# Optimization experiments

Measured on AMD Instinct MI355X. Metric: run time of the kernel, lower is better.

Reference implementation:

```python
import math
import jax, jax.numpy as jnp
import numpy as np

L, D, H, F, V, S = 4, 1024, 16, 4096, 50257, 2048
HS = D // H
EPS = 1e-5
STD = 0.02


def setup_inputs() -> dict:
    key = jax.random.key(0)
    keys = iter(jax.random.split(key, 24))

    def rn(shape):
        return (jax.random.normal(next(keys), shape, jnp.float32) * STD)

    inp = {
        "input_ids": jax.random.randint(next(keys), (1, S), 0, V, dtype=jnp.int64),
        "tok_emb": rn((V, D)),
        "pos_emb": rn((S, D)),
        # per-layer stacked params; linear weights stored [in, out]
        "Wq": rn((L, D, D)), "bq": jnp.zeros((L, D)),
        "Wk": rn((L, D, D)), "bk": jnp.zeros((L, D)),
        "Wv": rn((L, D, D)), "bv": jnp.zeros((L, D)),
        "Wo": rn((L, D, D)), "bo": jnp.zeros((L, D)),
        "W1": rn((L, D, F)), "b1": jnp.zeros((L, F)),
        "W2": rn((L, F, D)), "b2": jnp.zeros((L, D)),
        "ln1w": jnp.ones((L, D)), "ln1b": jnp.zeros((L, D)),
        "ln2w": jnp.ones((L, D)), "ln2b": jnp.zeros((L, D)),
        "lnfw": jnp.ones((D,)), "lnfb": jnp.zeros((D,)),
        "lm_head": rn((V, D)),  # torch Linear weight layout [out, in]
    }
    return inp


def _layernorm(x, w, b):
    m = jnp.mean(x, axis=-1, keepdims=True)
    v = jnp.mean(jnp.square(x - m), axis=-1, keepdims=True)
    return (x - m) * jax.lax.rsqrt(v + EPS) * w + b


def reference(input_ids, tok_emb, pos_emb, Wq, bq, Wk, bk, Wv, bv, Wo, bo,
              W1, b1, W2, b2, ln1w, ln1b, ln2w, ln2b, lnfw, lnfb, lm_head):
    B, Sq = input_ids.shape
    h = tok_emb[input_ids] + pos_emb[None, :Sq]  # [B,S,D]
    causal = jnp.tril(jnp.ones((Sq, Sq), dtype=bool))
    scale = 1.0 / math.sqrt(HS)

    def block(h, p):
        wq, bq_, wk, bk_, wv, bv_, wo, bo_, w1, b1_, w2, b2_, l1w, l1b, l2w, l2b = p
        x = _layernorm(h, l1w, l1b)
        q = (x @ wq + bq_).reshape(B, Sq, H, HS).transpose(0, 2, 1, 3)
        k = (x @ wk + bk_).reshape(B, Sq, H, HS).transpose(0, 2, 1, 3)
        v = (x @ wv + bv_).reshape(B, Sq, H, HS).transpose(0, 2, 1, 3)
        scores = jnp.einsum('bhqd,bhkd->bhqk', q, k) * scale
        scores = jnp.where(causal, scores, jnp.finfo(scores.dtype).min)
        attn = jax.nn.softmax(scores, axis=-1)  # dropout is identity at eval
        out = jnp.einsum('bhqk,bhkd->bhqd', attn, v)
        out = out.transpose(0, 2, 1, 3).reshape(B, Sq, D)
        h = h + out @ wo + bo_
        x = _layernorm(h, l2w, l2b)
        h = h + jax.nn.gelu(x @ w1 + b1_, approximate=False) @ w2 + b2_
        return h, None

    h, _ = jax.lax.scan(block, h, (Wq, bq, Wk, bk, Wv, bv, Wo, bo,
                                   W1, b1, W2, b2, ln1w, ln1b, ln2w, ln2b))
    h = _layernorm(h, lnfw, lnfb)
    logits = h @ lm_head.T  # [B,S,V]
    return logits
```

## Files before the change

kernel.cpp:

```cpp
#include <hip/hip_runtime.h>
#include <math.h>
#include <stdint.h>


#define SEQ 2048
#define DIM 1024
#define NHEAD 16
#define FFN 4096
#define VOCAB 50257
#define NLAYER 4
#define LNEPS 1e-5f
#define QKVD 3072
#define KVB 128

using bf16x8 = __attribute__((ext_vector_type(8))) short;
using s16x4  = __attribute__((ext_vector_type(4))) short;
using f32x4  = __attribute__((ext_vector_type(4))) float;
using fl4    = __attribute__((ext_vector_type(4))) float;

static __device__ __forceinline__ short f2bf(float f) {
  uint32_t u = __float_as_uint(f);
  u = (u + 0x7fffu + ((u >> 16) & 1u)) >> 16;
  return (short)u;
}
static __device__ __forceinline__ float bf2f(short s) {
  return __uint_as_float(((uint32_t)(uint16_t)s) << 16);
}
static __device__ __forceinline__ void gload_lds16(const void* g, void* l) {
  __builtin_amdgcn_global_load_lds((const __attribute__((address_space(1))) void*)g,
                                   (__attribute__((address_space(3))) void*)l, 16, 0, 0);
}

__global__ void embed_kernel(const int* __restrict__ ids,
                             const float* __restrict__ tok,
                             const float* __restrict__ pos,
                             float* __restrict__ h) {
  int i = blockIdx.x * blockDim.x + threadIdx.x;
  if (i < SEQ * DIM) {
    int s = i / DIM, d = i % DIM;
    h[i] = tok[(long)ids[s] * DIM + d] + pos[i];
  }
}

__global__ void ln_kernel(const float* __restrict__ x, const float* __restrict__ w,
                          const float* __restrict__ b, short* __restrict__ y) {
  int row = blockIdx.x;
  const float* xr = x + (long)row * DIM;
  short* yr = y + (long)row * DIM;
  int tid = threadIdx.x;
  float v0 = xr[tid], v1 = xr[tid + 256], v2 = xr[tid + 512], v3 = xr[tid + 768];
  __shared__ float red[8];
  float s = v0 + v1 + v2 + v3;
#pragma unroll
  for (int o = 32; o >= 1; o >>= 1) s += __shfl_xor(s, o);
  if ((tid & 63) == 0) red[tid >> 6] = s;
  __syncthreads();
  float mean = (red[0] + red[1] + red[2] + red[3]) * (1.f / DIM);
  float d0 = v0 - mean, d1 = v1 - mean, d2 = v2 - mean, d3 = v3 - mean;
  float q = d0 * d0 + d1 * d1 + d2 * d2 + d3 * d3;
#pragma unroll
  for (int o = 32; o >= 1; o >>= 1) q += __shfl_xor(q, o);
  if ((tid & 63) == 0) red[4 + (tid >> 6)] = q;
  __syncthreads();
  float var = (red[4] + red[5] + red[6] + red[7]) * (1.f / DIM);
  float rstd = rsqrtf(var + LNEPS);
  yr[tid]       = f2bf(d0 * rstd * w[tid] + b[tid]);
  yr[tid + 256] = f2bf(d1 * rstd * w[tid + 256] + b[tid + 256]);
  yr[tid + 512] = f2bf(d2 * rstd * w[tid + 512] + b[tid + 512]);
  yr[tid + 768] = f2bf(d3 * rstd * w[tid + 768] + b[tid + 768]);
}

__global__ void transpose_w(const float* __restrict__ in, short* __restrict__ out,
                            int K, int N) {
  __shared__ float t[32][33];
  int c0 = blockIdx.x * 32, r0 = blockIdx.y * 32;
  int tx = threadIdx.x & 31, ty = threadIdx.x >> 5;
#pragma unroll
  for (int i = 0; i < 4; i++)
    t[ty + i * 8][tx] = in[(long)(r0 + ty + i * 8) * N + c0 + tx];
  __syncthreads();
#pragma unroll
  for (int i = 0; i < 4; i++)
    out[(long)(c0 + ty + i * 8) * K + r0 + tx] = f2bf(t[tx][ty + i * 8]);
}

struct TW4 { const float* src[4]; short* dst[4]; };
__global__ void transpose_w4(TW4 p) {
  const float* in = p.src[blockIdx.z];
  short* out = p.dst[blockIdx.z];
  __shared__ float t[32][33];
  int c0 = blockIdx.x * 32, r0 = blockIdx.y * 32;
  int tx = threadIdx.x & 31, ty = threadIdx.x >> 5;
#pragma unroll
  for (int i = 0; i < 4; i++)
    t[ty + i * 8][tx] = in[(long)(r0 + ty + i * 8) * DIM + c0 + tx];
  __syncthreads();
#pragma unroll
  for (int i = 0; i < 4; i++)
    out[(long)(c0 + ty + i * 8) * DIM + r0 + tx] = f2bf(t[tx][ty + i * 8]);
}

__global__ void transpose_v(const short* __restrict__ qkv, short* __restrict__ vt) {
  __shared__ short t[64][72];
  int s0 = blockIdx.x * 64, c0 = blockIdx.y * 64;
  int tid = threadIdx.x;
#pragma unroll
  for (int i = 0; i < 2; i++) {
    int ca = i * 256 + tid;
    int row = ca >> 3, cp = ca & 7;
    bf16x8 v = *(const bf16x8*)(qkv + (long)(s0 + row) * QKVD + 2 * DIM + c0 + cp * 8);
    *(bf16x8*)&t[row][cp * 8] = v;
  }
  __syncthreads();
#pragma unroll
  for (int i = 0; i < 2; i++) {
    int ca = i * 256 + tid;
    int crow = ca >> 3, sp = ca & 7;
    s16x4 a, b;
#pragma unroll
    for (int u = 0; u < 4; u++) a[u] = t[sp * 8 + u][crow];
#pragma unroll
    for (int u = 0; u < 4; u++) b[u] = t[sp * 8 + 4 + u][crow];
    bf16x8 o;
#pragma unroll
    for (int u = 0; u < 4; u++) { o[u] = a[u]; o[4 + u] = b[u]; }
    *(bf16x8*)(vt + (long)(c0 + crow) * SEQ + s0 + sp * 8) = o;
  }
}

__global__ void conv_bf16(const float* __restrict__ in, short* __restrict__ out, long n4) {
  long i = (long)blockIdx.x * blockDim.x + threadIdx.x;
  long stride = (long)gridDim.x * blockDim.x;
  for (; i < n4; i += stride) {
    fl4 v = *(const fl4*)(in + i * 4);
    s16x4 o;
    o[0] = f2bf(v[0]); o[1] = f2bf(v[1]); o[2] = f2bf(v[2]); o[3] = f2bf(v[3]);
    *(s16x4*)(out + i * 4) = o;
  }
}

__global__ void bias_cat(const float* __restrict__ bq, const float* __restrict__ bk,
                         const float* __restrict__ bv, float* __restrict__ out) {
  int i = blockIdx.x * 256 + threadIdx.x;
  if (i < QKVD) out[i] = i < DIM ? bq[i] : (i < 2 * DIM ? bk[i - DIM] : bv[i - 2 * DIM]);
}

template <bool XCDSWZ>
__global__ __launch_bounds__(512, 2) void gemm256(
    const short* __restrict__ A, const short* __restrict__ Bt,
    float* __restrict__ C, int N, int K) {
  __shared__ short ldsA[2][256 * 64];
  __shared__ short ldsB[2][256 * 64];
  const int tid = threadIdx.x, wid = tid >> 6, lane = tid & 63;
  const int l16 = lane & 15, lg = lane >> 4;
  const int wm = wid >> 2, wn = wid & 3;
  int bx = blockIdx.x, by = blockIdx.y;
  if (XCDSWZ) {
    int gx = gridDim.x, nwg = gx * gridDim.y;
    int flat = by * gx + bx;
    int nf = (flat & 7) * (nwg >> 3) + (flat >> 3);
    bx = nf % gx; by = nf / gx;
  }
  const long m0 = (long)bx * 256, n0 = (long)by * 256;
  const int NT = K / 64;

  auto SA = [&](int t, int b, int r0) {
    int row = r0 + wid * 8 + (lane >> 3);
    int c = (lane & 7) ^ (row & 7);
    gload_lds16(A + (m0 + row) * (long)K + t * 64 + c * 8,
                &ldsA[b][(r0 + wid * 8) * 64]);
  };
  auto SB = [&](int t, int b, int r0) {
    int row = r0 + wid * 8 + (lane >> 3);
    int c = (lane & 7) ^ (row & 7);
    int rowb = (int)n0 + row;
    if (rowb > N - 1) rowb = N - 1;
    gload_lds16(Bt + (long)rowb * K + t * 64 + c * 8,
                &ldsB[b][(r0 + wid * 8) * 64]);
  };

  f32x4 acc[8][4] = {};
  bf16x8 bfr[4][2];

  auto PH = [&](int b, int q) {
    bf16x8 af[2][2];
    if (q == 0) {
#pragma unroll
      for (int nf = 0; nf < 4; nf++) {
        int row = wn * 64 + nf * 16 + l16;
#pragma unroll
        for (int ks = 0; ks < 2; ks++)
          bfr[nf][ks] = *(const bf16x8*)((const char*)&ldsB[b][0] + row * 128 +
                                         (((ks * 4 + lg) ^ (row & 7)) * 16));
      }
    }
#pragma unroll
    for (int j = 0; j < 2; j++) {
      int row = wm * 128 + (q * 2 + j) * 16 + l16;
#pragma unroll
      for (int ks = 0; ks < 2; ks++)
        af[j][ks] = *(const bf16x8*)((const char*)&ldsA[b][0] + row * 128 +
                                     (((ks * 4 + lg) ^ (row & 7)) * 16));
    }
    __builtin_amdgcn_s_barrier();
    __builtin_amdgcn_s_setprio(1);
#pragma unroll
    for (int ks = 0; ks < 2; ks++)
#pragma unroll
      for (int j = 0; j < 2; j++)
#pragma unroll
        for (int nf = 0; nf < 4; nf++)
          acc[q * 2 + j][nf] =
              __builtin_amdgcn_mfma_f32_16x16x32_bf16(af[j][ks], bfr[nf][ks],
                                                      acc[q * 2 + j][nf], 0, 0, 0);
    __builtin_amdgcn_s_setprio(0);
  };

  SA(0, 0, 0); SA(0, 0, 64); SA(0, 0, 128); SA(0, 0, 192);
  SB(0, 0, 0); SB(0, 0, 64); SB(0, 0, 128); SB(0, 0, 192);
  SA(1, 1, 0); SA(1, 1, 128);
  asm volatile("s_waitcnt vmcnt(2)" ::: "memory");
  __builtin_amdgcn_s_barrier();

  for (int i = 0; i < NT / 2; i++) {
    const int e = 2 * i, o = e + 1;
    const bool more = (e + 2) < NT;
    SA(o, 1, 64); SA(o, 1, 192);
    PH(0, 0);
    __builtin_amdgcn_s_barrier();
    SB(o, 1, 0); SB(o, 1, 64);
    PH(0, 1);
    __builtin_amdgcn_s_barrier();
    SB(o, 1, 128); SB(o, 1, 192);
    PH(0, 2);
    __builtin_amdgcn_s_barrier();
    if (more) { SA(e + 2, 0, 0); SA(e + 2, 0, 128); }
    PH(0, 3);
    if (more) asm volatile("s_waitcnt vmcnt(2)" ::: "memory");
    else      asm volatile("s_waitcnt vmcnt(0)" ::: "memory");
    __builtin_amdgcn_s_barrier();
    if (more) { SA(e + 2, 0, 64); SA(e + 2, 0, 192); }
    PH(1, 0);
    __builtin_amdgcn_s_barrier();
    if (more) { SB(e + 2, 0, 0); SB(e + 2, 0, 64); }
    PH(1, 1);
    __builtin_amdgcn_s_barrier();
    if (more) { SB(e + 2, 0, 128); SB(e + 2, 0, 192); }
    PH(1, 2);
    __builtin_amdgcn_s_barrier();
    if (more) { SA(e + 3, 1, 0); SA(e + 3, 1, 128); }
    PH(1, 3);
    if (more) {
      asm volatile("s_waitcnt vmcnt(2)" ::: "memory");
      __builtin_amdgcn_s_barrier();
    }
  }

#pragma unroll
  for (int mf = 0; mf < 8; mf++)
#pragma unroll
    for (int nf = 0; nf < 4; nf++)
#pragma unroll
      for (int r = 0; r < 4; r++) {
        long row = m0 + wm * 128 + mf * 16 + lg * 4 + r;
        long col = n0 + wn * 64 + nf * 16 + l16;
        if (col < N) C[row * (long)N + col] = acc[mf][nf][r];
      }
}

template <bool GELU, bool RES, bool BIAS, bool OUTBF16, int KS, bool XCDSWZ>
__global__ __launch_bounds__(256, 3) void gemm4(
    const short* __restrict__ A, const short* __restrict__ Bt,
    const float* __restrict__ bias, const float* __restrict__ res,
    void* __restrict__ Cout, int N, int Kfull) {
  __shared__ short lds[3][(128 + 128) * 32];
  const int tid = threadIdx.x, wid = tid >> 6, lane = tid & 63;
  const int l16 = lane & 15, lg = lane >> 4;
  int bx = blockIdx.x, by = blockIdx.y;
  if (XCDSWZ) {
    int gx = gridDim.x, nwg = gx * gridDim.y;
    int flat = by * gx + bx;
    int nf = (flat & 7) * (nwg >> 3) + (flat >> 3);
    bx = nf % gx; by = nf / gx;
  }
  const long m0 = (long)bx * 128, n0 = (long)by * 128;
  const int K = Kfull / KS;
  const int kbase = blockIdx.z * K;
  const int NT = K / 32;
  const int wr = (wid >> 1) * 64, wc = (wid & 1) * 64;

#define STAGE4(t, b)                                                            \
  {                                                                             \
    short* As_ = lds[b];                                                        \
    short* Bs_ = lds[b] + 128 * 32;                                             \
    int kk_ = kbase + (t) * 32;                                                 \
    _Pragma("unroll")                                                           \
    for (int i_ = 0; i_ < 2; i_++) {                                            \
      int ca_ = i_ * 256 + tid;                                                 \
      int row_ = ca_ >> 2, cp_ = ca_ & 3, c_ = cp_ ^ ((row_ >> 1) & 3);         \
      gload_lds16(A + (m0 + row_) * (long)Kfull + kk_ + c_ * 8,                 \
                  As_ + (i_ * 256 + wid * 64) * 8);                             \
    }                                                                           \
    _Pragma("unroll")                                                           \
    for (int i_ = 0; i_ < 2; i_++) {                                            \
      int ca_ = i_ * 256 + tid;                                                 \
      int row_ = ca_ >> 2, cp_ = ca_ & 3, c_ = cp_ ^ ((row_ >> 1) & 3);         \
      int rowb_ = (int)n0 + row_;                                               \
      if (rowb_ > N - 1) rowb_ = N - 1;                                         \
      gload_lds16(Bt + (long)rowb_ * Kfull + kk_ + c_ * 8,                      \
                  Bs_ + (i_ * 256 + wid * 64) * 8);                             \
    }                                                                           \
  }

  f32x4 acc[4][4] = {};
  STAGE4(0, 0);
  STAGE4(1, 1);
  asm volatile("s_waitcnt vmcnt(4)" ::: "memory");
  __builtin_amdgcn_s_barrier();
  __builtin_amdgcn_sched_barrier(0);

  for (int t = 0; t < NT; t++) {
    const int b = t % 3;
    if (t + 2 < NT) STAGE4(t + 2, (t + 2) % 3);
    const short* As = lds[b];
    const short* Bs = lds[b] + 128 * 32;
    bf16x8 af[4], bfr[4];
#pragma unroll
    for (int m = 0; m < 4; m++) {
      int row = wr + m * 16 + l16;
      af[m] = *(const bf16x8*)((const char*)As + row * 64 + ((lg ^ ((row >> 1) & 3)) * 16));
    }
#pragma unroll
    for (int n = 0; n < 4; n++) {
      int row = wc + n * 16 + l16;
      bfr[n] = *(const bf16x8*)((const char*)Bs + row * 64 + ((lg ^ ((row >> 1) & 3)) * 16));
    }
    __builtin_amdgcn_s_setprio(1);
#pragma unroll
    for (int m = 0; m < 4; m++)
#pragma unroll
      for (int n = 0; n < 4; n++)
        acc[m][n] = __builtin_amdgcn_mfma_f32_16x16x32_bf16(af[m], bfr[n], acc[m][n], 0, 0, 0);
    __builtin_amdgcn_s_setprio(0);
    if (t + 2 < NT) {
      asm volatile("s_waitcnt vmcnt(4)" ::: "memory");
    } else if (t + 1 < NT) {
      asm volatile("s_waitcnt vmcnt(0)" ::: "memory");
    }
    if (t + 1 < NT) {
      __builtin_amdgcn_s_barrier();
      __builtin_amdgcn_sched_barrier(0);
    }
  }
#undef STAGE4

  const int lr4 = lg * 4;
  if (KS == 1) {
#pragma unroll
    for (int m = 0; m < 4; m++)
#pragma unroll
      for (int n = 0; n < 4; n++)
#pragma unroll
        for (int r = 0; r < 4; r++) {
          long row = m0 + wr + m * 16 + lr4 + r;
          long col = n0 + wc + n * 16 + l16;
          if (col < N) {
            float v = acc[m][n][r];
            if (BIAS) v += bias[col];
            if (GELU) v = 0.5f * v * (1.f + erff(v * 0.70710678118f));
            if (RES) v += res[row * (long)N + col];
            if (OUTBF16) ((short*)Cout)[row * (long)N + col] = f2bf(v);
            else ((float*)Cout)[row * (long)N + col] = v;
          }
        }
  } else {
    long M = (long)gridDim.x * 128;
    float* P = (float*)Cout + (long)blockIdx.z * M * N;
#pragma unroll
    for (int m = 0; m < 4; m++)
#pragma unroll
      for (int n = 0; n < 4; n++)
#pragma unroll
        for (int r = 0; r < 4; r++) {
          long row = m0 + wr + m * 16 + lr4 + r;
          long col = n0 + wc + n * 16 + l16;
          P[row * (long)N + col] = acc[m][n][r];
        }
  }
}

template <int KS>
__global__ void reduce_k(const float* __restrict__ part, const float* __restrict__ bias,
                         float* __restrict__ h, int N, long MN) {
  long i = ((long)blockIdx.x * 256 + threadIdx.x) * 4;
  if (i >= MN) return;
  fl4 s = *(const fl4*)(h + i);
  fl4 b = *(const fl4*)(bias + (int)(i % N));
  s[0] += b[0]; s[1] += b[1]; s[2] += b[2]; s[3] += b[3];
#pragma unroll
  for (int ks = 0; ks < KS; ks++) {
    fl4 p = *(const fl4*)(part + (long)ks * MN + i);
    s[0] += p[0]; s[1] += p[1]; s[2] += p[2]; s[3] += p[3];
  }
  *(fl4*)(h + i) = s;
}

__global__ __launch_bounds__(256) void attn_mfma(const short* __restrict__ qkv,
                                                 const short* __restrict__ vtg,
                                                 short* __restrict__ Oa) {
  int hh = blockIdx.x, qb = blockIdx.y;
  int q0 = qb * 64;
  int tid = threadIdx.x, wv = tid >> 6, lane = tid & 63;
  int l16 = lane & 15, lg = lane >> 4;
  int hcol = hh * 64;
  __shared__ short Ks[KVB * 64];
  __shared__ short Vt[64 * KVB];
  __shared__ short Pl[4][16 * KVB];

  bf16x8 qf[2];
  {
    const short* qrow = qkv + (long)(q0 + wv * 16 + l16) * QKVD + hcol;
#pragma unroll
    for (int dc = 0; dc < 2; dc++) {
      bf16x8 t = *(const bf16x8*)(qrow + dc * 32 + lg * 8);
#pragma unroll
      for (int j = 0; j < 8; j++) t[j] = f2bf(bf2f(t[j]) * 0.125f);
      qf[dc] = t;
    }
  }
  f32x4 of[4] = {};
  float mrun[4], lrun[4];
#pragma unroll
  for (int r = 0; r < 4; r++) { mrun[r] = -3e38f; lrun[r] = 0.f; }

  int nt = qb / 2 + 1;
  for (int kt = 0; kt < nt; kt++) {
    int k0 = kt * KVB;
    __syncthreads();
#pragma unroll
    for (int i = 0; i < 4; i++) {
      int ca = i * 256 + tid;
      int row = ca >> 3, cp = ca & 7, c = cp ^ (row & 7);
      int ldsoff = (i * 256 + wv * 64) * 8;
      gload_lds16(qkv + (long)(k0 + row) * QKVD + DIM + hcol + c * 8, (short*)Ks + ldsoff);
    }
#pragma unroll
    for (int i = 0; i < 4; i++) {
      int ca = i * 256 + tid;
      int row = ca >> 4, cp = ca & 15, c = cp ^ (row & 7);
      int ldsoff = (i * 256 + wv * 64) * 8;
      gload_lds16(vtg + (long)(hcol + row) * SEQ + k0 + c * 8, (short*)Vt + ldsoff);
    }
    __syncthreads();

    f32x4 sacc[8] = {};
#pragma unroll
    for (int kc = 0; kc < 8; kc++) {
      int row = kc * 16 + l16;
#pragma unroll
      for (int dc = 0; dc < 2; dc++) {
        bf16x8 kf = *(const bf16x8*)((const char*)Ks + row * 128 + (((dc * 4 + lg) ^ (row & 7)) * 16));
        sacc[kc] = __builtin_amdgcn_mfma_f32_16x16x32_bf16(qf[dc], kf, sacc[kc], 0, 0, 0);
      }
    }

    float sv[8][4], pf[8][4];
#pragma unroll
    for (int kc = 0; kc < 8; kc++)
#pragma unroll
      for (int r = 0; r < 4; r++) sv[kc][r] = sacc[kc][r];
    if (kt == nt - 1) {
#pragma unroll
      for (int kc = 0; kc < 8; kc++)
#pragma unroll
        for (int r = 0; r < 4; r++) {
          int kg = k0 + kc * 16 + l16;
          int rg = q0 + wv * 16 + lg * 4 + r;
          if (kg > rg) sv[kc][r] = -3e38f;
        }
    }
    float corr[4];
#pragma unroll
    for (int r = 0; r < 4; r++) {
      float m01 = fmaxf(sv[0][r], sv[1][r]), m23 = fmaxf(sv[2][r], sv[3][r]);
      float m45 = fmaxf(sv[4][r], sv[5][r]), m67 = fmaxf(sv[6][r], sv[7][r]);
      float mt = fmaxf(fmaxf(m01, m23), fmaxf(m45, m67));
#pragma unroll
      for (int o = 8; o >= 1; o >>= 1) mt = fmaxf(mt, __shfl_xor(mt, o));
      float mn = fmaxf(mrun[r], mt);
      corr[r] = __expf(mrun[r] - mn);
      mrun[r] = mn;
      float ps = 0.f;
#pragma unroll
      for (int kc = 0; kc < 8; kc++) {
        float p = __expf(sv[kc][r] - mn);
        pf[kc][r] = p;
        ps += p;
      }
#pragma unroll
      for (int o = 8; o >= 1; o >>= 1) ps += __shfl_xor(ps, o);
      lrun[r] = lrun[r] * corr[r] + ps;
    }
#pragma unroll
    for (int c = 0; c < 4; c++)
#pragma unroll
      for (int r = 0; r < 4; r++) of[c][r] *= corr[r];
#pragma unroll
    for (int kc = 0; kc < 8; kc++)
#pragma unroll
      for (int r = 0; r < 4; r++) {
        int row = lg * 4 + r, col = kc * 16 + l16;
        int chunk = col >> 3;
        *(short*)((char*)Pl[wv] + row * 256 + ((chunk ^ (row & 7)) * 16) + (col & 7) * 2) = f2bf(pf[kc][r]);
      }
    bf16x8 pfr[4];
#pragma unroll
    for (int kc2 = 0; kc2 < 4; kc2++) {
      int cl = kc2 * 4 + lg;
      pfr[kc2] = *(const bf16x8*)((const char*)Pl[wv] + l16 * 256 + ((cl ^ (l16 & 7)) * 16));
    }
#pragma unroll
    for (int c = 0; c < 4; c++)
#pragma unroll
      for (int kc2 = 0; kc2 < 4; kc2++) {
        int vrow = c * 16 + l16;
        int cl = kc2 * 4 + lg;
        bf16x8 vf = *(const bf16x8*)((const char*)Vt + vrow * 256 + ((cl ^ (vrow & 7)) * 16));
        of[c] = __builtin_amdgcn_mfma_f32_16x16x32_bf16(pfr[kc2], vf, of[c], 0, 0, 0);
      }
  }
#pragma unroll
  for (int c = 0; c < 4; c++)
#pragma unroll
    for (int r = 0; r < 4; r++) {
      int rowg = q0 + wv * 16 + lg * 4 + r;
      int colg = hcol + c * 16 + l16;
      Oa[(long)rowg * DIM + colg] = f2bf(of[c][r] / lrun[r]);
    }
}

extern "C" void kernel_launch(void* const* d_in, const int* in_sizes, int n_in,
                              void* d_out, int out_size, void* d_ws, size_t ws_size,
                              hipStream_t stream) {
  const int* ids = (const int*)d_in[0];
  const float* tok = (const float*)d_in[1];
  const float* pos = (const float*)d_in[2];
  const float* Wq = (const float*)d_in[3];
  const float* bq = (const float*)d_in[4];
  const float* Wk = (const float*)d_in[5];
  const float* bk = (const float*)d_in[6];
  const float* Wv = (const float*)d_in[7];
  const float* bv = (const float*)d_in[8];
  const float* Wo = (const float*)d_in[9];
  const float* bo = (const float*)d_in[10];
  const float* W1 = (const float*)d_in[11];
  const float* b1 = (const float*)d_in[12];
  const float* W2 = (const float*)d_in[13];
  const float* b2 = (const float*)d_in[14];
  const float* ln1w = (const float*)d_in[15];
  const float* ln1b = (const float*)d_in[16];
  const float* ln2w = (const float*)d_in[17];
  const float* ln2b = (const float*)d_in[18];
  const float* lnfw = (const float*)d_in[19];
  const float* lnfb = (const float*)d_in[20];
  const float* lmh = (const float*)d_in[21];
  float* out = (float*)d_out;

  char* wsb = (char*)d_ws;
  float* h = (float*)wsb;
  short* x = (short*)(wsb + 8388608);
  char* big = wsb + 8388608 + 4194304;
  short* qkv  = (short*)big;
  short* a    = (short*)(big + 12582912);
  short* vt   = (short*)(big + 16777216);
  short* fbuf = (short*)(big + 20971520);
  float* pproj = (float*)fbuf;
  float* pffn2 = (float*)big;
  char* wdyn = big + 37748736;
  short* wqkvT = (short*)wdyn;
  short* woT   = (short*)(wdyn + 6291456);
  short* w1T   = (short*)(wdyn + 8388608);
  short* w2T   = (short*)(wdyn + 16777216);
  float* bias3 = (float*)(wdyn + 25165824);
  short* lmhB = (short*)big;

  const long MN = (long)SEQ * DIM;

  embed_kernel<<<(SEQ * DIM + 255) / 256, 256, 0, stream>>>(ids, tok, pos, h);

  dim3 gQKV(SEQ / 128, QKVD / 128);
  dim3 gPROJ(SEQ / 128, DIM / 128, 2);
  dim3 gFFN1(SEQ / 128, FFN / 128);
  dim3 gFFN2(SEQ / 128, DIM / 128, 2);
  dim3 gV(SEQ / 256, (VOCAB + 255) / 256);

  for (int l = 0; l < NLAYER; l++) {
    TW4 tw;
    tw.src[0] = Wq + (long)l * DIM * DIM; tw.dst[0] = wqkvT;
    tw.src[1] = Wk + (long)l * DIM * DIM; tw.dst[1] = wqkvT + (long)DIM * DIM;
    tw.src[2] = Wv + (long)l * DIM * DIM; tw.dst[2] = wqkvT + (long)2 * DIM * DIM;
    tw.src[3] = Wo + (long)l * DIM * DIM; tw.dst[3] = woT;
    transpose_w4<<<dim3(32, 32, 4), 256, 0, stream>>>(tw);
    transpose_w<<<dim3(128, 32), 256, 0, stream>>>(W1 + (long)l * DIM * FFN, w1T, DIM, FFN);
    transpose_w<<<dim3(32, 128), 256, 0, stream>>>(W2 + (long)l * FFN * DIM, w2T, FFN, DIM);
    bias_cat<<<12, 256, 0, stream>>>(bq + (long)l * DIM, bk + (long)l * DIM, bv + (long)l * DIM, bias3);

    ln_kernel<<<SEQ, 256, 0, stream>>>(h, ln1w + (long)l * DIM, ln1b + (long)l * DIM, x);
    gemm4<false, false, true, true, 1, true><<<gQKV, 256, 0, stream>>>(x, wqkvT, bias3, nullptr, qkv, QKVD, DIM);
    transpose_v<<<dim3(SEQ / 64, DIM / 64), 256, 0, stream>>>(qkv, vt);
    attn_mfma<<<dim3(NHEAD, SEQ / 64), 256, 0, stream>>>(qkv, vt, a);
    gemm4<false, false, false, false, 2, true><<<gPROJ, 256, 0, stream>>>(a, woT, nullptr, nullptr, pproj, DIM, DIM);
    reduce_k<2><<<(int)(MN / 1024), 256, 0, stream>>>(pproj, bo + (long)l * DIM, h, DIM, MN);
    ln_kernel<<<SEQ, 256, 0, stream>>>(h, ln2w + (long)l * DIM, ln2b + (long)l * DIM, x);
    gemm4<true, false, true, true, 1, true><<<gFFN1, 256, 0, stream>>>(x, w1T, b1 + (long)l * FFN, nullptr, fbuf, FFN, DIM);
    gemm4<false, false, false, false, 2, true><<<gFFN2, 256, 0, stream>>>(fbuf, w2T, nullptr, nullptr, pffn2, DIM, FFN);
    reduce_k<2><<<(int)(MN / 1024), 256, 0, stream>>>(pffn2, b2 + (long)l * DIM, h, DIM, MN);
  }

  ln_kernel<<<SEQ, 256, 0, stream>>>(h, lnfw, lnfb, x);
  conv_bf16<<<2048, 256, 0, stream>>>(lmh, lmhB, (long)VOCAB * DIM / 4);
  gemm256<true><<<gV, 512, 0, stream>>>(x, lmhB, out, VOCAB, DIM);
}
```

Before: 1.150 ms.

## Fuse split-K reduce with LayerNorm, add 64-row GEMM, double-buffer attention KV

```diff
diff --git a/kernel.cpp b/kernel.cpp
--- a/kernel.cpp
+++ b/kernel.cpp
@@ -70,34 +70,91 @@
   yr[tid + 768] = f2bf(d3 * rstd * w[tid + 768] + b[tid + 768]);
 }
 
-__global__ void transpose_w(const float* __restrict__ in, short* __restrict__ out,
+__global__ void reduce_ln(const float* __restrict__ part, const float* __restrict__ bias,
+                          const float* __restrict__ lnw, const float* __restrict__ lnb,
+                          float* __restrict__ h, short* __restrict__ x) {
+  const long MN = (long)SEQ * DIM;
+  int row = blockIdx.x, tid = threadIdx.x;
+  long off = (long)row * DIM + tid * 4;
+  fl4 hv = *(const fl4*)(h + off);
+  fl4 p0 = *(const fl4*)(part + off);
+  fl4 p1 = *(const fl4*)(part + MN + off);
+  fl4 bv = *(const fl4*)(bias + tid * 4);
+  float v[4];
+#pragma unroll
+  for (int u = 0; u < 4; u++) v[u] = hv[u] + p0[u] + p1[u] + bv[u];
+  __shared__ float red[8];
+  float s = v[0] + v[1] + v[2] + v[3];
+#pragma unroll
+  for (int o = 32; o >= 1; o >>= 1) s += __shfl_xor(s, o);
+  if ((tid & 63) == 0) red[tid >> 6] = s;
+  __syncthreads();
+  float mean = (red[0] + red[1] + red[2] + red[3]) * (1.f / DIM);
+  float d[4], q = 0.f;
+#pragma unroll
+  for (int u = 0; u < 4; u++) { d[u] = v[u] - mean; q += d[u] * d[u]; }
+#pragma unroll
+  for (int o = 32; o >= 1; o >>= 1) q += __shfl_xor(q, o);
+  if ((tid & 63) == 0) red[4 + (tid >> 6)] = q;
+  fl4 hw; hw[0] = v[0]; hw[1] = v[1]; hw[2] = v[2]; hw[3] = v[3];
+  *(fl4*)(h + off) = hw;
+  __syncthreads();
+  float var = (red[4] + red[5] + red[6] + red[7]) * (1.f / DIM);
+  float rstd = rsqrtf(var + LNEPS);
+  fl4 w = *(const fl4*)(lnw + tid * 4);
+  fl4 bb = *(const fl4*)(lnb + tid * 4);
+  s16x4 o;
+#pragma unroll
+  for (int u = 0; u < 4; u++) o[u] = f2bf(d[u] * rstd * w[u] + bb[u]);
+  *(s16x4*)(x + off) = o;
+}
+
+__global__ void transpose64(const float* __restrict__ in, short* __restrict__ out,
                             int K, int N) {
-  __shared__ float t[32][33];
-  int c0 = blockIdx.x * 32, r0 = blockIdx.y * 32;
-  int tx = threadIdx.x & 31, ty = threadIdx.x >> 5;
-#pragma unroll
-  for (int i = 0; i < 4; i++)
-    t[ty + i * 8][tx] = in[(long)(r0 + ty + i * 8) * N + c0 + tx];
+  __shared__ float ts[64][65];
+  int c0 = blockIdx.x * 64, r0 = blockIdx.y * 64;
+  int tid = threadIdx.x;
+  int lr = tid >> 4, lc4 = (tid & 15) * 4;
+#pragma unroll
+  for (int i = 0; i < 4; i++) {
+    fl4 v = *(const fl4*)(in + (long)(r0 + lr + i * 16) * N + c0 + lc4);
+    ts[lr + i * 16][lc4] = v[0]; ts[lr + i * 16][lc4 + 1] = v[1];
+    ts[lr + i * 16][lc4 + 2] = v[2]; ts[lr + i * 16][lc4 + 3] = v[3];
+  }
   __syncthreads();
 #pragma unroll
-  for (int i = 0; i < 4; i++)
-    out[(long)(c0 + ty + i * 8) * K + r0 + tx] = f2bf(t[tx][ty + i * 8]);
+  for (int i = 0; i < 2; i++) {
+    int oc = (tid >> 3) + i * 32, seg = tid & 7;
+    bf16x8 o;
+#pragma unroll
+    for (int u = 0; u < 8; u++) o[u] = f2bf(ts[seg * 8 + u][oc]);
+    *(bf16x8*)(out + (long)(c0 + oc) * K + r0 + seg * 8) = o;
+  }
 }
 
 struct TW4 { const float* src[4]; short* dst[4]; };
-__global__ void transpose_w4(TW4 p) {
+__global__ void transpose64_b4(TW4 p) {
   const float* in = p.src[blockIdx.z];
   short* out = p.dst[blockIdx.z];
-  __shared__ float t[32][33];
-  int c0 = blockIdx.x * 32, r0 = blockIdx.y * 32;
-  int tx = threadIdx.x & 31, ty = threadIdx.x >> 5;
-#pragma unroll
-  for (int i = 0; i < 4; i++)
-    t[ty + i * 8][tx] = in[(long)(r0 + ty + i * 8) * DIM + c0 + tx];
+  __shared__ float ts[64][65];
+  int c0 = blockIdx.x * 64, r0 = blockIdx.y * 64;
+  int tid = threadIdx.x;
+  int lr = tid >> 4, lc4 = (tid & 15) * 4;
+#pragma unroll
+  for (int i = 0; i < 4; i++) {
+    fl4 v = *(const fl4*)(in + (long)(r0 + lr + i * 16) * DIM + c0 + lc4);
+    ts[lr + i * 16][lc4] = v[0]; ts[lr + i * 16][lc4 + 1] = v[1];
+    ts[lr + i * 16][lc4 + 2] = v[2]; ts[lr + i * 16][lc4 + 3] = v[3];
+  }
   __syncthreads();
 #pragma unroll
-  for (int i = 0; i < 4; i++)
-    out[(long)(c0 + ty + i * 8) * DIM + r0 + tx] = f2bf(t[tx][ty + i * 8]);
+  for (int i = 0; i < 2; i++) {
+    int oc = (tid >> 3) + i * 32, seg = tid & 7;
+    bf16x8 o;
+#pragma unroll
+    for (int u = 0; u < 8; u++) o[u] = f2bf(ts[seg * 8 + u][oc]);
+    *(bf16x8*)(out + (long)(c0 + oc) * DIM + r0 + seg * 8) = o;
+  }
 }
 
 __global__ void transpose_v(const short* __restrict__ qkv, short* __restrict__ vt) {
@@ -116,14 +173,9 @@
   for (int i = 0; i < 2; i++) {
     int ca = i * 256 + tid;
     int crow = ca >> 3, sp = ca & 7;
-    s16x4 a, b;
-#pragma unroll
-    for (int u = 0; u < 4; u++) a[u] = t[sp * 8 + u][crow];
-#pragma unroll
-    for (int u = 0; u < 4; u++) b[u] = t[sp * 8 + 4 + u][crow];
     bf16x8 o;
 #pragma unroll
-    for (int u = 0; u < 4; u++) { o[u] = a[u]; o[4 + u] = b[u]; }
+    for (int u = 0; u < 8; u++) o[u] = t[sp * 8 + u][crow];
     *(bf16x8*)(vt + (long)(c0 + crow) * SEQ + s0 + sp * 8) = o;
   }
 }
@@ -143,6 +195,217 @@
                          const float* __restrict__ bv, float* __restrict__ out) {
   int i = blockIdx.x * 256 + threadIdx.x;
   if (i < QKVD) out[i] = i < DIM ? bq[i] : (i < 2 * DIM ? bk[i - DIM] : bv[i - 2 * DIM]);
+}
+
+template <bool GELU, bool BIAS, bool OUTBF16, int KS, bool XCDSWZ>
+__global__ __launch_bounds__(256, 4) void gemm_small(
+    const short* __restrict__ A, const short* __restrict__ Bt,
+    const float* __restrict__ bias, void* __restrict__ Cout, int N, int Kfull) {
+  __shared__ short lds[3][(64 + 128) * 32];
+  const int tid = threadIdx.x, wid = tid >> 6, lane = tid & 63;
+  const int l16 = lane & 15, lg = lane >> 4;
+  int bx = blockIdx.x, by = blockIdx.y;
+  if (XCDSWZ) {
+    int gx = gridDim.x, nwg = gx * gridDim.y;
+    int flat = by * gx + bx;
+    int nf = (flat & 7) * (nwg >> 3) + (flat >> 3);
+    bx = nf % gx; by = nf / gx;
+  }
+  const long m0 = (long)bx * 64, n0 = (long)by * 128;
+  const int K = Kfull / KS;
+  const int kbase = blockIdx.z * K;
+  const int NT = K / 32;
+  const int wm = wid >> 1, wn = wid & 1;
+
+#define STG(t, b)                                                               \
+  {                                                                             \
+    short* As_ = lds[b];                                                        \
+    short* Bs_ = lds[b] + 64 * 32;                                              \
+    int kk_ = kbase + (t) * 32;                                                 \
+    {                                                                           \
+      int row_ = tid >> 2, cp_ = tid & 3, c_ = cp_ ^ ((row_ >> 1) & 3);         \
+      gload_lds16(A + (m0 + row_) * (long)Kfull + kk_ + c_ * 8,                 \
+                  As_ + (wid * 64) * 8);                                        \
+    }                                                                           \
+    _Pragma("unroll")                                                           \
+    for (int i_ = 0; i_ < 2; i_++) {                                            \
+      int ca_ = i_ * 256 + tid;                                                 \
+      int row_ = ca_ >> 2, cp_ = ca_ & 3, c_ = cp_ ^ ((row_ >> 1) & 3);         \
+      gload_lds16(Bt + (long)(n0 + row_) * Kfull + kk_ + c_ * 8,                \
+                  Bs_ + (i_ * 256 + wid * 64) * 8);                             \
+    }                                                                           \
+  }
+
+  f32x4 acc[2][4] = {};
+  STG(0, 0);
+  STG(1, 1);
+  asm volatile("s_waitcnt vmcnt(3)" ::: "memory");
+  __builtin_amdgcn_s_barrier();
+  __builtin_amdgcn_sched_barrier(0);
+
+  for (int t = 0; t < NT; t++) {
+    const int b = t % 3;
+    if (t + 2 < NT) STG(t + 2, (t + 2) % 3);
+    const short* As = lds[b];
+    const short* Bs = lds[b] + 64 * 32;
+    bf16x8 af[2], bfr[4];
+#pragma unroll
+    for (int m = 0; m < 2; m++) {
+      int row = wm * 32 + m * 16 + l16;
+      af[m] = *(const bf16x8*)((const char*)As + row * 64 + ((lg ^ ((row >> 1) & 3)) * 16));
+    }
+#pragma unroll
+    for (int n = 0; n < 4; n++) {
+      int row = wn * 64 + n * 16 + l16;
+      bfr[n] = *(const bf16x8*)((const char*)Bs + row * 64 + ((lg ^ ((row >> 1) & 3)) * 16));
+    }
+    __builtin_amdgcn_s_setprio(1);
+#pragma unroll
+    for (int m = 0; m < 2; m++)
+#pragma unroll
+      for (int n = 0; n < 4; n++)
+        acc[m][n] = __builtin_amdgcn_mfma_f32_16x16x32_bf16(af[m], bfr[n], acc[m][n], 0, 0, 0);
+    __builtin_amdgcn_s_setprio(0);
+    if (t + 2 < NT) {
+      asm volatile("s_waitcnt vmcnt(3)" ::: "memory");
+    } else if (t + 1 < NT) {
+      asm volatile("s_waitcnt vmcnt(0)" ::: "memory");
+    }
+    if (t + 1 < NT) {
+      __builtin_amdgcn_s_barrier();
+      __builtin_amdgcn_sched_barrier(0);
+    }
+  }
+#undef STG
+
+  const int lr4 = lg * 4;
+  if (KS == 1) {
+#pragma unroll
+    for (int m = 0; m < 2; m++)
+#pragma unroll
+      for (int n = 0; n < 4; n++)
+#pragma unroll
+        for (int r = 0; r < 4; r++) {
+          long row = m0 + wm * 32 + m * 16 + lr4 + r;
+          long col = n0 + wn * 64 + n * 16 + l16;
+          float v = acc[m][n][r];
+          if (BIAS) v += bias[col];
+          if (GELU) v = 0.5f * v * (1.f + erff(v * 0.70710678118f));
+          if (OUTBF16) ((short*)Cout)[row * (long)N + col] = f2bf(v);
+          else ((float*)Cout)[row * (long)N + col] = v;
+        }
+  } else {
+    long M = (long)gridDim.x * 64;
+    float* P = (float*)Cout + (long)blockIdx.z * M * N;
+#pragma unroll
+    for (int m = 0; m < 2; m++)
+#pragma unroll
+      for (int n = 0; n < 4; n++)
+#pragma unroll
+        for (int r = 0; r < 4; r++) {
+          long row = m0 + wm * 32 + m * 16 + lr4 + r;
+          long col = n0 + wn * 64 + n * 16 + l16;
+          P[row * (long)N + col] = acc[m][n][r];
+        }
+  }
+}
+
+template <bool GELU, bool BIAS, bool OUTBF16, bool XCDSWZ>
+__global__ __launch_bounds__(256, 3) void gemm4(
+    const short* __restrict__ A, const short* __restrict__ Bt,
+    const float* __restrict__ bias, void* __restrict__ Cout, int N, int Kfull) {
+  __shared__ short lds[3][(128 + 128) * 32];
+  const int tid = threadIdx.x, wid = tid >> 6, lane = tid & 63;
+  const int l16 = lane & 15, lg = lane >> 4;
+  int bx = blockIdx.x, by = blockIdx.y;
+  if (XCDSWZ) {
+    int gx = gridDim.x, nwg = gx * gridDim.y;
+    int flat = by * gx + bx;
+    int nf = (flat & 7) * (nwg >> 3) + (flat >> 3);
+    bx = nf % gx; by = nf / gx;
+  }
+  const long m0 = (long)bx * 128, n0 = (long)by * 128;
+  const int NT = Kfull / 32;
+  const int wr = (wid >> 1) * 64, wc = (wid & 1) * 64;
+
+#define STAGE4(t, b)                                                            \
+  {                                                                             \
+    short* As_ = lds[b];                                                        \
+    short* Bs_ = lds[b] + 128 * 32;                                             \
+    int kk_ = (t) * 32;                                                         \
+    _Pragma("unroll")                                                           \
+    for (int i_ = 0; i_ < 2; i_++) {                                            \
+      int ca_ = i_ * 256 + tid;                                                 \
+      int row_ = ca_ >> 2, cp_ = ca_ & 3, c_ = cp_ ^ ((row_ >> 1) & 3);         \
+      gload_lds16(A + (m0 + row_) * (long)Kfull + kk_ + c_ * 8,                 \
+                  As_ + (i_ * 256 + wid * 64) * 8);                             \
+    }                                                                           \
+    _Pragma("unroll")                                                           \
+    for (int i_ = 0; i_ < 2; i_++) {                                            \
+      int ca_ = i_ * 256 + tid;                                                 \
+      int row_ = ca_ >> 2, cp_ = ca_ & 3, c_ = cp_ ^ ((row_ >> 1) & 3);         \
+      gload_lds16(Bt + (long)(n0 + row_) * Kfull + kk_ + c_ * 8,                \
+                  Bs_ + (i_ * 256 + wid * 64) * 8);                             \
+    }                                                                           \
+  }
+
+  f32x4 acc[4][4] = {};
+  STAGE4(0, 0);
+  STAGE4(1, 1);
+  asm volatile("s_waitcnt vmcnt(4)" ::: "memory");
+  __builtin_amdgcn_s_barrier();
+  __builtin_amdgcn_sched_barrier(0);
+
+  for (int t = 0; t < NT; t++) {
+    const int b = t % 3;
+    if (t + 2 < NT) STAGE4(t + 2, (t + 2) % 3);
+    const short* As = lds[b];
+    const short* Bs = lds[b] + 128 * 32;
+    bf16x8 af[4], bfr[4];
+#pragma unroll
+    for (int m = 0; m < 4; m++) {
+      int row = wr + m * 16 + l16;
+      af[m] = *(const bf16x8*)((const char*)As + row * 64 + ((lg ^ ((row >> 1) & 3)) * 16));
+    }
+#pragma unroll
+    for (int n = 0; n < 4; n++) {
+      int row = wc + n * 16 + l16;
+      bfr[n] = *(const bf16x8*)((const char*)Bs + row * 64 + ((lg ^ ((row >> 1) & 3)) * 16));
+    }
+    __builtin_amdgcn_s_setprio(1);
+#pragma unroll
+    for (int m = 0; m < 4; m++)
+#pragma unroll
+      for (int n = 0; n < 4; n++)
+        acc[m][n] = __builtin_amdgcn_mfma_f32_16x16x32_bf16(af[m], bfr[n], acc[m][n], 0, 0, 0);
+    __builtin_amdgcn_s_setprio(0);
+    if (t + 2 < NT) {
+      asm volatile("s_waitcnt vmcnt(4)" ::: "memory");
+    } else if (t + 1 < NT) {
+      asm volatile("s_waitcnt vmcnt(0)" ::: "memory");
+    }
+    if (t + 1 < NT) {
+      __builtin_amdgcn_s_barrier();
+      __builtin_amdgcn_sched_barrier(0);
+    }
+  }
+#undef STAGE4
+
+  const int lr4 = lg * 4;
+#pragma unroll
+  for (int m = 0; m < 4; m++)
+#pragma unroll
+    for (int n = 0; n < 4; n++)
+#pragma unroll
+      for (int r = 0; r < 4; r++) {
+        long row = m0 + wr + m * 16 + lr4 + r;
+        long col = n0 + wc + n * 16 + l16;
+        float v = acc[m][n][r];
+        if (BIAS) v += bias[col];
+        if (GELU) v = 0.5f * v * (1.f + erff(v * 0.70710678118f));
+        if (OUTBF16) ((short*)Cout)[row * (long)N + col] = f2bf(v);
+        else ((float*)Cout)[row * (long)N + col] = v;
+      }
 }
 
 template <bool XCDSWZ>
@@ -268,143 +531,6 @@
       }
 }
 
-template <bool GELU, bool RES, bool BIAS, bool OUTBF16, int KS, bool XCDSWZ>
-__global__ __launch_bounds__(256, 3) void gemm4(
-    const short* __restrict__ A, const short* __restrict__ Bt,
-    const float* __restrict__ bias, const float* __restrict__ res,
-    void* __restrict__ Cout, int N, int Kfull) {
-  __shared__ short lds[3][(128 + 128) * 32];
-  const int tid = threadIdx.x, wid = tid >> 6, lane = tid & 63;
-  const int l16 = lane & 15, lg = lane >> 4;
-  int bx = blockIdx.x, by = blockIdx.y;
-  if (XCDSWZ) {
-    int gx = gridDim.x, nwg = gx * gridDim.y;
-    int flat = by * gx + bx;
-    int nf = (flat & 7) * (nwg >> 3) + (flat >> 3);
-    bx = nf % gx; by = nf / gx;
-  }
-  const long m0 = (long)bx * 128, n0 = (long)by * 128;
-  const int K = Kfull / KS;
-  const int kbase = blockIdx.z * K;
-  const int NT = K / 32;
-  const int wr = (wid >> 1) * 64, wc = (wid & 1) * 64;
-
-#define STAGE4(t, b)                                                            \
-  {                                                                             \
-    short* As_ = lds[b];                                                        \
-    short* Bs_ = lds[b] + 128 * 32;                                             \
-    int kk_ = kbase + (t) * 32;                                                 \
-    _Pragma("unroll")                                                           \
-    for (int i_ = 0; i_ < 2; i_++) {                                            \
-      int ca_ = i_ * 256 + tid;                                                 \
-      int row_ = ca_ >> 2, cp_ = ca_ & 3, c_ = cp_ ^ ((row_ >> 1) & 3);         \
-      gload_lds16(A + (m0 + row_) * (long)Kfull + kk_ + c_ * 8,                 \
-                  As_ + (i_ * 256 + wid * 64) * 8);                             \
-    }                                                                           \
-    _Pragma("unroll")                                                           \
-    for (int i_ = 0; i_ < 2; i_++) {                                            \
-      int ca_ = i_ * 256 + tid;                                                 \
-      int row_ = ca_ >> 2, cp_ = ca_ & 3, c_ = cp_ ^ ((row_ >> 1) & 3);         \
-      int rowb_ = (int)n0 + row_;                                               \
-      if (rowb_ > N - 1) rowb_ = N - 1;                                         \
-      gload_lds16(Bt + (long)rowb_ * Kfull + kk_ + c_ * 8,                      \
-                  Bs_ + (i_ * 256 + wid * 64) * 8);                             \
-    }                                                                           \
-  }
-
-  f32x4 acc[4][4] = {};
-  STAGE4(0, 0);
-  STAGE4(1, 1);
-  asm volatile("s_waitcnt vmcnt(4)" ::: "memory");
-  __builtin_amdgcn_s_barrier();
-  __builtin_amdgcn_sched_barrier(0);
-
-  for (int t = 0; t < NT; t++) {
-    const int b = t % 3;
-    if (t + 2 < NT) STAGE4(t + 2, (t + 2) % 3);
-    const short* As = lds[b];
-    const short* Bs = lds[b] + 128 * 32;
-    bf16x8 af[4], bfr[4];
-#pragma unroll
-    for (int m = 0; m < 4; m++) {
-      int row = wr + m * 16 + l16;
-      af[m] = *(const bf16x8*)((const char*)As + row * 64 + ((lg ^ ((row >> 1) & 3)) * 16));
-    }
-#pragma unroll
-    for (int n = 0; n < 4; n++) {
-      int row = wc + n * 16 + l16;
-      bfr[n] = *(const bf16x8*)((const char*)Bs + row * 64 + ((lg ^ ((row >> 1) & 3)) * 16));
-    }
-    __builtin_amdgcn_s_setprio(1);
-#pragma unroll
-    for (int m = 0; m < 4; m++)
-#pragma unroll
-      for (int n = 0; n < 4; n++)
-        acc[m][n] = __builtin_amdgcn_mfma_f32_16x16x32_bf16(af[m], bfr[n], acc[m][n], 0, 0, 0);
-    __builtin_amdgcn_s_setprio(0);
-    if (t + 2 < NT) {
-      asm volatile("s_waitcnt vmcnt(4)" ::: "memory");
-    } else if (t + 1 < NT) {
-      asm volatile("s_waitcnt vmcnt(0)" ::: "memory");
-    }
-    if (t + 1 < NT) {
-      __builtin_amdgcn_s_barrier();
-      __builtin_amdgcn_sched_barrier(0);
-    }
-  }
-#undef STAGE4
-
-  const int lr4 = lg * 4;
-  if (KS == 1) {
-#pragma unroll
-    for (int m = 0; m < 4; m++)
-#pragma unroll
-      for (int n = 0; n < 4; n++)
-#pragma unroll
-        for (int r = 0; r < 4; r++) {
-          long row = m0 + wr + m * 16 + lr4 + r;
-          long col = n0 + wc + n * 16 + l16;
-          if (col < N) {
-            float v = acc[m][n][r];
-            if (BIAS) v += bias[col];
-            if (GELU) v = 0.5f * v * (1.f + erff(v * 0.70710678118f));
-            if (RES) v += res[row * (long)N + col];
-            if (OUTBF16) ((short*)Cout)[row * (long)N + col] = f2bf(v);
-            else ((float*)Cout)[row * (long)N + col] = v;
-          }
-        }
-  } else {
-    long M = (long)gridDim.x * 128;
-    float* P = (float*)Cout + (long)blockIdx.z * M * N;
-#pragma unroll
-    for (int m = 0; m < 4; m++)
-#pragma unroll
-      for (int n = 0; n < 4; n++)
-#pragma unroll
-        for (int r = 0; r < 4; r++) {
-          long row = m0 + wr + m * 16 + lr4 + r;
-          long col = n0 + wc + n * 16 + l16;
-          P[row * (long)N + col] = acc[m][n][r];
-        }
-  }
-}
-
-template <int KS>
-__global__ void reduce_k(const float* __restrict__ part, const float* __restrict__ bias,
-                         float* __restrict__ h, int N, long MN) {
-  long i = ((long)blockIdx.x * 256 + threadIdx.x) * 4;
-  if (i >= MN) return;
-  fl4 s = *(const fl4*)(h + i);
-  fl4 b = *(const fl4*)(bias + (int)(i % N));
-  s[0] += b[0]; s[1] += b[1]; s[2] += b[2]; s[3] += b[3];
-#pragma unroll
-  for (int ks = 0; ks < KS; ks++) {
-    fl4 p = *(const fl4*)(part + (long)ks * MN + i);
-    s[0] += p[0]; s[1] += p[1]; s[2] += p[2]; s[3] += p[3];
-  }
-  *(fl4*)(h + i) = s;
-}
-
 __global__ __launch_bounds__(256) void attn_mfma(const short* __restrict__ qkv,
                                                  const short* __restrict__ vtg,
                                                  short* __restrict__ Oa) {
@@ -413,8 +539,8 @@
   int tid = threadIdx.x, wv = tid >> 6, lane = tid & 63;
   int l16 = lane & 15, lg = lane >> 4;
   int hcol = hh * 64;
-  __shared__ short Ks[KVB * 64];
-  __shared__ short Vt[64 * KVB];
+  __shared__ short Ks[2][KVB * 64];
+  __shared__ short Vt[2][64 * KVB];
   __shared__ short Pl[4][16 * KVB];
 
   bf16x8 qf[2];
@@ -433,25 +559,34 @@
 #pragma unroll
   for (int r = 0; r < 4; r++) { mrun[r] = -3e38f; lrun[r] = 0.f; }
 
+#define STAGEKV(kt_, b_)                                                        \
+  {                                                                             \
+    int k0_ = (kt_) * KVB;                                                      \
+    _Pragma("unroll")                                                           \
+    for (int i = 0; i < 4; i++) {                                               \
+      int ca = i * 256 + tid;                                                   \
+      int row = ca >> 3, cp = ca & 7, c = cp ^ (row & 7);                       \
+      gload_lds16(qkv + (long)(k0_ + row) * QKVD + DIM + hcol + c * 8,          \
+                  (short*)Ks[b_] + (i * 256 + wv * 64) * 8);                    \
+    }                                                                           \
+    _Pragma("unroll")                                                           \
+    for (int i = 0; i < 4; i++) {                                               \
+      int ca = i * 256 + tid;                                                   \
+      int row = ca >> 4, cp = ca & 15, c = cp ^ (row & 7);                      \
+      gload_lds16(vtg + (long)(hcol + row) * SEQ + k0_ + c * 8,                 \
+                  (short*)Vt[b_] + (i * 256 + wv * 64) * 8);                    \
+    }                                                                           \
+  }
+
   int nt = qb / 2 + 1;
+  STAGEKV(0, 0);
+  asm volatile("s_waitcnt vmcnt(0)" ::: "memory");
+  __builtin_amdgcn_s_barrier();
+
   for (int kt = 0; kt < nt; kt++) {
+    const int cur = kt & 1;
+    if (kt + 1 < nt) STAGEKV(kt + 1, cur ^ 1);
     int k0 = kt * KVB;
-    __syncthreads();
-#pragma unroll
-    for (int i = 0; i < 4; i++) {
-      int ca = i * 256 + tid;
-      int row = ca >> 3, cp = ca & 7, c = cp ^ (row & 7);
-      int ldsoff = (i * 256 + wv * 64) * 8;
-      gload_lds16(qkv + (long)(k0 + row) * QKVD + DIM + hcol + c * 8, (short*)Ks + ldsoff);
-    }
-#pragma unroll
-    for (int i = 0; i < 4; i++) {
-      int ca = i * 256 + tid;
-      int row = ca >> 4, cp = ca & 15, c = cp ^ (row & 7);
-      int ldsoff = (i * 256 + wv * 64) * 8;
-      gload_lds16(vtg + (long)(hcol + row) * SEQ + k0 + c * 8, (short*)Vt + ldsoff);
-    }
-    __syncthreads();
 
     f32x4 sacc[8] = {};
 #pragma unroll
@@ -459,7 +594,7 @@
       int row = kc * 16 + l16;
 #pragma unroll
       for (int dc = 0; dc < 2; dc++) {
-        bf16x8 kf = *(const bf16x8*)((const char*)Ks + row * 128 + (((dc * 4 + lg) ^ (row & 7)) * 16));
+        bf16x8 kf = *(const bf16x8*)((const char*)Ks[cur] + row * 128 + (((dc * 4 + lg) ^ (row & 7)) * 16));
         sacc[kc] = __builtin_amdgcn_mfma_f32_16x16x32_bf16(qf[dc], kf, sacc[kc], 0, 0, 0);
       }
     }
@@ -525,10 +660,16 @@
       for (int kc2 = 0; kc2 < 4; kc2++) {
         int vrow = c * 16 + l16;
         int cl = kc2 * 4 + lg;
-        bf16x8 vf = *(const bf16x8*)((const char*)Vt + vrow * 256 + ((cl ^ (vrow & 7)) * 16));
+        bf16x8 vf = *(const bf16x8*)((const char*)Vt[cur] + vrow * 256 + ((cl ^ (vrow & 7)) * 16));
         of[c] = __builtin_amdgcn_mfma_f32_16x16x32_bf16(pfr[kc2], vf, of[c], 0, 0, 0);
       }
-  }
+    if (kt + 1 < nt) {
+      asm volatile("s_waitcnt vmcnt(0)" ::: "memory");
+      __builtin_amdgcn_s_barrier();
+      __builtin_amdgcn_sched_barrier(0);
+    }
+  }
+#undef STAGEKV
 #pragma unroll
   for (int c = 0; c < 4; c++)
 #pragma unroll
@@ -584,14 +725,13 @@
   float* bias3 = (float*)(wdyn + 25165824);
   short* lmhB = (short*)big;
 
-  const long MN = (long)SEQ * DIM;
-
   embed_kernel<<<(SEQ * DIM + 255) / 256, 256, 0, stream>>>(ids, tok, pos, h);
-
-  dim3 gQKV(SEQ / 128, QKVD / 128);
-  dim3 gPROJ(SEQ / 128, DIM / 128, 2);
+  ln_kernel<<<SEQ, 256, 0, stream>>>(h, ln1w, ln1b, x);
+
+  dim3 gQKV(SEQ / 64, QKVD / 128);
+  dim3 gPROJ(SEQ / 64, DIM / 128, 2);
   dim3 gFFN1(SEQ / 128, FFN / 128);
-  dim3 gFFN2(SEQ / 128, DIM / 128, 2);
+  dim3 gFFN2(SEQ / 64, DIM / 128, 2);
   dim3 gV(SEQ / 256, (VOCAB + 255) / 256);
 
   for (int l = 0; l < NLAYER; l++) {
@@ -600,24 +740,24 @@
     tw.src[1] = Wk + (long)l * DIM * DIM; tw.dst[1] = wqkvT + (long)DIM * DIM;
     tw.src[2] = Wv + (long)l * DIM * DIM; tw.dst[2] = wqkvT + (long)2 * DIM * DIM;
     tw.src[3] = Wo + (long)l * DIM * DIM; tw.dst[3] = woT;
-    transpose_w4<<<dim3(32, 32, 4), 256, 0, stream>>>(tw);
-    transpose_w<<<dim3(128, 32), 256, 0, stream>>>(W1 + (long)l * DIM * FFN, w1T, DIM, FFN);
-    transpose_w<<<dim3(32, 128), 256, 0, stream>>>(W2 + (long)l * FFN * DIM, w2T, FFN, DIM);
+    transpose64_b4<<<dim3(16, 16, 4), 256, 0, stream>>>(tw);
+    transpose64<<<dim3(64, 16), 256, 0, stream>>>(W1 + (long)l * DIM * FFN, w1T, DIM, FFN);
+    transpose64<<<dim3(16, 64), 256, 0, stream>>>(W2 + (long)l * FFN * DIM, w2T, FFN, DIM);
     bias_cat<<<12, 256, 0, stream>>>(bq + (long)l * DIM, bk + (long)l * DIM, bv + (long)l * DIM, bias3);
 
-    ln_kernel<<<SEQ, 256, 0, stream>>>(h, ln1w + (long)l * DIM, ln1b + (long)l * DIM, x);
-    gemm4<false, false, true, true, 1, true><<<gQKV, 256, 0, stream>>>(x, wqkvT, bias3, nullptr, qkv, QKVD, DIM);
+    gemm_small<false, true, true, 1, true><<<gQKV, 256, 0, stream>>>(x, wqkvT, bias3, qkv, QKVD, DIM);
     transpose_v<<<dim3(SEQ / 64, DIM / 64), 256, 0, stream>>>(qkv, vt);
     attn_mfma<<<dim3(NHEAD, SEQ / 64), 256, 0, stream>>>(qkv, vt, a);
-    gemm4<false, false, false, false, 2, true><<<gPROJ, 256, 0, stream>>>(a, woT, nullptr, nullptr, pproj, DIM, DIM);
-    reduce_k<2><<<(int)(MN / 1024), 256, 0, stream>>>(pproj, bo + (long)l * DIM, h, DIM, MN);
-    ln_kernel<<<SEQ, 256, 0, stream>>>(h, ln2w + (long)l * DIM, ln2b + (long)l * DIM, x);
-    gemm4<true, false, true, true, 1, true><<<gFFN1, 256, 0, stream>>>(x, w1T, b1 + (long)l * FFN, nullptr, fbuf, FFN, DIM);
-    gemm4<false, false, false, false, 2, true><<<gFFN2, 256, 0, stream>>>(fbuf, w2T, nullptr, nullptr, pffn2, DIM, FFN);
-    reduce_k<2><<<(int)(MN / 1024), 256, 0, stream>>>(pffn2, b2 + (long)l * DIM, h, DIM, MN);
-  }
-
-  ln_kernel<<<SEQ, 256, 0, stream>>>(h, lnfw, lnfb, x);
+    gemm_small<false, false, false, 2, true><<<gPROJ, 256, 0, stream>>>(a, woT, nullptr, pproj, DIM, DIM);
+    reduce_ln<<<SEQ, 256, 0, stream>>>(pproj, bo + (long)l * DIM,
+                                       ln2w + (long)l * DIM, ln2b + (long)l * DIM, h, x);
+    gemm4<true, true, true, true><<<gFFN1, 256, 0, stream>>>(x, w1T, b1 + (long)l * FFN, fbuf, FFN, DIM);
+    gemm_small<false, false, false, 2, true><<<gFFN2, 256, 0, stream>>>(fbuf, w2T, nullptr, pffn2, DIM, FFN);
+    const float* nw = (l < NLAYER - 1) ? ln1w + (long)(l + 1) * DIM : lnfw;
+    const float* nb = (l < NLAYER - 1) ? ln1b + (long)(l + 1) * DIM : lnfb;
+    reduce_ln<<<SEQ, 256, 0, stream>>>(pffn2, b2 + (long)l * DIM, nw, nb, h, x);
+  }
+
   conv_bf16<<<2048, 256, 0, stream>>>(lmh, lmhB, (long)VOCAB * DIM / 4);
   gemm256<true><<<gV, 512, 0, stream>>>(x, lmhB, out, VOCAB, DIM);
 }
```

Measured after the change: 1.138 ms. No clear change (-1.0%).
